# Kernel tuning notes

Hardware: AMD Instinct MI355X
Metric: run time of the kernel (lower is better)

## Reference

```python
import jax, jax.numpy as jnp
import numpy as np
import math

B, P = 4096, 512
WDT = 10          # lyr_wdt = number of irreps (multiplicity)
EPS2 = 1e-12      # NormActivation epsilon=1e-6, squared


def setup_inputs() -> dict:
    key = jax.random.key(0)
    ks = jax.random.split(key, 8)
    return {
        "invar_2b": jax.random.normal(ks[0], (B, P, 5), jnp.float32),
        "vectors_2b": jax.random.normal(ks[1], (B, P, 9), jnp.float32),
        # torch.nn.Linear params (stored as [in, out])
        "w1_0": jax.random.normal(ks[2], (5, WDT), jnp.float32) / math.sqrt(5.0),
        "b1_0": jnp.zeros((WDT,), jnp.float32),
        "w1_1": jax.random.normal(ks[3], (WDT, WDT), jnp.float32) / math.sqrt(float(WDT)),
        "b1_1": jnp.zeros((WDT,), jnp.float32),
        # o3.Linear weights (N(0,1) init, e3nn normalizes by sqrt(mul_in) in forward)
        "lin0_w": jax.random.normal(ks[4], (3, WDT), jnp.float32),
        "na0_b": jnp.zeros((WDT,), jnp.float32),   # NormActivation bias
        "lin1_w": jax.random.normal(ks[5], (WDT, WDT), jnp.float32),
        "na1_b": jnp.zeros((WDT,), jnp.float32),
        "final_w": jax.random.normal(ks[6], (WDT, 1), jnp.float32),
    }


def _self_intrc(x, w, bias):
    """o3.Linear (mul_in x 1o -> mul_out x 1o) + NormActivation(tanh, eps=1e-6, bias).

    x: [B, P, mul_in, 3]
    """
    mul_in = x.shape[-2]
    # single l=1 -> l=1 path; e3nn o3.Linear scales by 1/sqrt(fan_in)
    y = jnp.einsum('bpuc,uw->bpwc', x, w) / jnp.sqrt(jnp.float32(mul_in))
    # NormActivation: norm per irrep, clamped at eps^2 before sqrt
    n = jnp.sqrt(jnp.maximum(jnp.sum(y * y, axis=-1), EPS2))  # [B,P,mul_out]
    s = jnp.tanh(n + bias) / n                                # act(norm+b)/norm
    return y * s[..., None]


def reference(invar_2b, vectors_2b, w1_0, b1_0, w1_1, b1_1,
              lin0_w, na0_b, lin1_w, na1_b, final_w):
    # scalar branch: Linear(5,10) + ReLU, Linear(10,10) + ReLU
    y = jax.nn.relu(invar_2b @ w1_0 + b1_0)
    y = jax.nn.relu(y @ w1_1 + b1_1)              # [B, P, WDT] (10x0e)

    # equivariant branch: two self_intrc blocks on 3x1o -> 10x1o -> 10x1o
    v = vectors_2b.reshape(B, P, 3, 3)            # [B,P,3 irreps,3 comps]
    x = _self_intrc(v, lin0_w, na0_b)             # [B,P,WDT,3]
    x = _self_intrc(x, lin1_w, na1_b)             # [B,P,WDT,3]

    # ElementwiseTensorProduct(10x0e, 10x1o) -> 10x1o: per-irrep scalar gating
    x = y[..., None] * x                          # [B,P,WDT,3]

    # final o3.Linear 10x1o -> 1x1o
    x = jnp.einsum('bpuc,uw->bpwc', x, final_w) / jnp.sqrt(jnp.float32(WDT))
    return jnp.sum(x[..., 0, :], axis=1)          # sum over pairs -> [B, 3]
```

## Files before the change

kernel.cpp:

```cpp
#include <hip/hip_runtime.h>
#include <math.h>

#define BB 4096
#define PP 512
#define WDT 10

typedef float float2v __attribute__((ext_vector_type(2)));

#define PKFMA(a, b, c) __builtin_elementwise_fma(a, b, c)
#define PKMAX(a, b)    __builtin_elementwise_max(a, b)
#define FENCE()        __builtin_amdgcn_sched_barrier(0)

__device__ __forceinline__ float2v bc2(float s) { return (float2v){s, s}; }

__device__ __forceinline__ float fast_tanh(float x) {
    float e = __builtin_amdgcn_exp2f(x * 2.8853900817779268f);
    return 1.0f - 2.0f * __builtin_amdgcn_rcpf(e + 1.0f);
}

__global__ __launch_bounds__(256) void frc_2b_kernel(
    const float* __restrict__ invar,
    const float* __restrict__ vectors,
    const float* __restrict__ w1_0,
    const float* __restrict__ b1_0,
    const float* __restrict__ w1_1,
    const float* __restrict__ b1_1,
    const float* __restrict__ lin0_w,
    const float* __restrict__ na0_b,
    const float* __restrict__ lin1_w,
    const float* __restrict__ na1_b,
    const float* __restrict__ final_w,
    float* __restrict__ out)
{
    __shared__ float red[4][3];

    const int b   = blockIdx.x;
    const int tid = threadIdx.x;

    const float* iv0 = invar   + ((size_t)b * PP + tid) * 5;
    const float* vv0 = vectors + ((size_t)b * PP + tid) * 9;
    float in5a[2][5];
    float v[2][9];
    #pragma unroll
    for (int i = 0; i < 5; ++i) { in5a[0][i] = iv0[i]; in5a[1][i] = iv0[256 * 5 + i]; }
    #pragma unroll
    for (int i = 0; i < 9; ++i) { v[0][i] = vv0[i]; v[1][i] = vv0[256 * 9 + i]; }

    const float k3sq  = 0.33333333333333333f;
    const float k3k10 = 0.18257418583505536f;
    const float k10   = 0.31622776601683794f;
    const float2v z2  = {0.f, 0.f};

    float2v yp[2][5];
    #pragma unroll
    for (int jp = 0; jp < 5; ++jp) {
        float2v bb = *(const float2v*)(b1_0 + 2 * jp);
        yp[0][jp] = bb; yp[1][jp] = bb;
    }
    #pragma unroll
    for (int i = 0; i < 5; ++i) {
        #pragma unroll
        for (int jp = 0; jp < 5; ++jp) {
            float2v wp = *(const float2v*)(w1_0 + i * WDT + 2 * jp);
            yp[0][jp] = PKFMA(wp, bc2(in5a[0][i]), yp[0][jp]);
            yp[1][jp] = PKFMA(wp, bc2(in5a[1][i]), yp[1][jp]);
        }
    }
    #pragma unroll
    for (int pr = 0; pr < 2; ++pr)
        #pragma unroll
        for (int jp = 0; jp < 5; ++jp) yp[pr][jp] = PKMAX(yp[pr][jp], z2);
    FENCE();

    float2v y2p[2][5];
    #pragma unroll
    for (int jp = 0; jp < 5; ++jp) {
        float2v bb = *(const float2v*)(b1_1 + 2 * jp);
        y2p[0][jp] = bb; y2p[1][jp] = bb;
    }
    #pragma unroll
    for (int k = 0; k < 5; ++k) {
        #pragma unroll
        for (int jp = 0; jp < 5; ++jp) {
            float2v wp = *(const float2v*)(w1_1 + k * WDT + 2 * jp);
            y2p[0][jp] = PKFMA(wp, bc2(yp[0][k >> 1][k & 1]), y2p[0][jp]);
            y2p[1][jp] = PKFMA(wp, bc2(yp[1][k >> 1][k & 1]), y2p[1][jp]);
        }
    }
    FENCE();
    #pragma unroll
    for (int k = 5; k < WDT; ++k) {
        #pragma unroll
        for (int jp = 0; jp < 5; ++jp) {
            float2v wp = *(const float2v*)(w1_1 + k * WDT + 2 * jp);
            y2p[0][jp] = PKFMA(wp, bc2(yp[0][k >> 1][k & 1]), y2p[0][jp]);
            y2p[1][jp] = PKFMA(wp, bc2(yp[1][k >> 1][k & 1]), y2p[1][jp]);
        }
    }
    #pragma unroll
    for (int pr = 0; pr < 2; ++pr)
        #pragma unroll
        for (int jp = 0; jp < 5; ++jp) y2p[pr][jp] = PKMAX(y2p[pr][jp], z2);
    FENCE();

    float2v c0p[2][5], c1p[2][5], c2p[2][5];
    #pragma unroll
    for (int pr = 0; pr < 2; ++pr)
        #pragma unroll
        for (int jp = 0; jp < 5; ++jp) { c0p[pr][jp] = z2; c1p[pr][jp] = z2; c2p[pr][jp] = z2; }
    #pragma unroll
    for (int u = 0; u < 3; ++u) {
        #pragma unroll
        for (int jp = 0; jp < 5; ++jp) {
            float2v wp = *(const float2v*)(lin0_w + u * WDT + 2 * jp);
            #pragma unroll
            for (int pr = 0; pr < 2; ++pr) {
                c0p[pr][jp] = PKFMA(wp, bc2(v[pr][u * 3 + 0]), c0p[pr][jp]);
                c1p[pr][jp] = PKFMA(wp, bc2(v[pr][u * 3 + 1]), c1p[pr][jp]);
                c2p[pr][jp] = PKFMA(wp, bc2(v[pr][u * 3 + 2]), c2p[pr][jp]);
            }
        }
    }
    float2v x0p[2][5], x1p[2][5], x2p[2][5];
    #pragma unroll
    for (int jp = 0; jp < 5; ++jp) {
        float2v nab = *(const float2v*)(na0_b + 2 * jp);
        #pragma unroll
        for (int pr = 0; pr < 2; ++pr) {
            float2v n2p = PKFMA(c0p[pr][jp], c0p[pr][jp],
                          PKFMA(c1p[pr][jp], c1p[pr][jp], c2p[pr][jp] * c2p[pr][jp]));
            float2v mp  = PKMAX(n2p * bc2(k3sq), bc2(1e-12f));
            float fh[2];
            #pragma unroll
            for (int h = 0; h < 2; ++h) {
                float m     = mp[h];
                float inv_n = __builtin_amdgcn_rsqf(m);
                float n     = m * inv_n;
                float t     = fast_tanh(n + nab[h]);
                fh[h] = t * inv_n * k3k10;
            }
            float2v fp = {fh[0], fh[1]};
            x0p[pr][jp] = c0p[pr][jp] * fp;
            x1p[pr][jp] = c1p[pr][jp] * fp;
            x2p[pr][jp] = c2p[pr][jp] * fp;
        }
    }
    FENCE();

    float2v e0p[2][5], e1p[2][5], e2p[2][5];
    #pragma unroll
    for (int pr = 0; pr < 2; ++pr)
        #pragma unroll
        for (int jp = 0; jp < 5; ++jp) { e0p[pr][jp] = z2; e1p[pr][jp] = z2; e2p[pr][jp] = z2; }
    #pragma unroll
    for (int u = 0; u < 5; ++u) {
        #pragma unroll
        for (int jp = 0; jp < 5; ++jp) {
            float2v wp = *(const float2v*)(lin1_w + u * WDT + 2 * jp);
            #pragma unroll
            for (int pr = 0; pr < 2; ++pr) {
                e0p[pr][jp] = PKFMA(wp, bc2(x0p[pr][u >> 1][u & 1]), e0p[pr][jp]);
                e1p[pr][jp] = PKFMA(wp, bc2(x1p[pr][u >> 1][u & 1]), e1p[pr][jp]);
                e2p[pr][jp] = PKFMA(wp, bc2(x2p[pr][u >> 1][u & 1]), e2p[pr][jp]);
            }
        }
    }
    FENCE();
    #pragma unroll
    for (int u = 5; u < WDT; ++u) {
        #pragma unroll
        for (int jp = 0; jp < 5; ++jp) {
            float2v wp = *(const float2v*)(lin1_w + u * WDT + 2 * jp);
            #pragma unroll
            for (int pr = 0; pr < 2; ++pr) {
                e0p[pr][jp] = PKFMA(wp, bc2(x0p[pr][u >> 1][u & 1]), e0p[pr][jp]);
                e1p[pr][jp] = PKFMA(wp, bc2(x1p[pr][u >> 1][u & 1]), e1p[pr][jp]);
                e2p[pr][jp] = PKFMA(wp, bc2(x2p[pr][u >> 1][u & 1]), e2p[pr][jp]);
            }
        }
    }
    FENCE();

    float2v a0p = z2, a1p = z2, a2p = z2;
    #pragma unroll
    for (int jp = 0; jp < 5; ++jp) {
        float2v nab = *(const float2v*)(na1_b + 2 * jp);
        float2v fwp = *(const float2v*)(final_w + 2 * jp);
        #pragma unroll
        for (int pr = 0; pr < 2; ++pr) {
            float2v n2p = PKFMA(e0p[pr][jp], e0p[pr][jp],
                          PKFMA(e1p[pr][jp], e1p[pr][jp], e2p[pr][jp] * e2p[pr][jp]));
            float2v mp  = PKMAX(n2p, bc2(1e-12f));
            float gh[2];
            #pragma unroll
            for (int h = 0; h < 2; ++h) {
                float m     = mp[h];
                float inv_n = __builtin_amdgcn_rsqf(m);
                float n     = m * inv_n;
                float t     = fast_tanh(n + nab[h]);
                gh[h] = y2p[pr][jp][h] * t * inv_n * fwp[h];
            }
            float2v gp = {gh[0], gh[1]};
            a0p = PKFMA(e0p[pr][jp], gp, a0p);
            a1p = PKFMA(e1p[pr][jp], gp, a1p);
            a2p = PKFMA(e2p[pr][jp], gp, a2p);
        }
    }
    float acc0 = (a0p[0] + a0p[1]) * k10;
    float acc1 = (a1p[0] + a1p[1]) * k10;
    float acc2 = (a2p[0] + a2p[1]) * k10;

    #pragma unroll
    for (int off = 32; off > 0; off >>= 1) {
        acc0 += __shfl_down(acc0, off, 64);
        acc1 += __shfl_down(acc1, off, 64);
        acc2 += __shfl_down(acc2, off, 64);
    }
    const int wave = tid >> 6;
    if ((tid & 63) == 0) { red[wave][0] = acc0; red[wave][1] = acc1; red[wave][2] = acc2; }
    __syncthreads();
    if (tid == 0) {
        float r0 = 0.f, r1 = 0.f, r2 = 0.f;
        #pragma unroll
        for (int wv = 0; wv < 4; ++wv) { r0 += red[wv][0]; r1 += red[wv][1]; r2 += red[wv][2]; }
        out[b * 3 + 0] = r0;
        out[b * 3 + 1] = r1;
        out[b * 3 + 2] = r2;
    }
}

extern "C" void kernel_launch(void* const* d_in, const int* in_sizes, int n_in,
                              void* d_out, int out_size, void* d_ws, size_t ws_size,
                              hipStream_t stream) {
    const float* invar   = (const float*)d_in[0];
    const float* vectors = (const float*)d_in[1];
    const float* w1_0    = (const float*)d_in[2];
    const float* b1_0    = (const float*)d_in[3];
    const float* w1_1    = (const float*)d_in[4];
    const float* b1_1    = (const float*)d_in[5];
    const float* lin0_w  = (const float*)d_in[6];
    const float* na0_b   = (const float*)d_in[7];
    const float* lin1_w  = (const float*)d_in[8];
    const float* na1_b   = (const float*)d_in[9];
    const float* final_w = (const float*)d_in[10];
    float* out = (float*)d_out;

    frc_2b_kernel<<<BB, 256, 0, stream>>>(invar, vectors, w1_0, b1_0, w1_1, b1_1,
                                          lin0_w, na0_b, lin1_w, na1_b, final_w, out);
}
```

Baseline: 166.4 us.

## Process four contiguous pairs per thread with 128-bit vector loads

Each thread now handles four adjacent pairs instead of two strided ones, and the block shrinks to 128 threads. The contiguous layout lets every thread read its 20 invariant floats and 36 vector floats as float4 loads, which cuts the number of load instructions. The cost is roughly double the per-thread register state, which may lower occupancy. Per-lane 16-byte strided accesses also coalesce less well across a wave.

```diff
diff --git a/kernel.cpp b/kernel.cpp
--- a/kernel.cpp
+++ b/kernel.cpp
@@ -4,8 +4,11 @@
 #define BB 4096
 #define PP 512
 #define WDT 10
+#define NP 4
+#define NT 128
 
 typedef float float2v __attribute__((ext_vector_type(2)));
+typedef float float4v __attribute__((ext_vector_type(4)));
 
 #define PKFMA(a, b, c) __builtin_elementwise_fma(a, b, c)
 #define PKMAX(a, b)    __builtin_elementwise_max(a, b)
@@ -18,7 +21,7 @@
     return 1.0f - 2.0f * __builtin_amdgcn_rcpf(e + 1.0f);
 }
 
-__global__ __launch_bounds__(256) void frc_2b_kernel(
+__global__ __launch_bounds__(NT) void frc_2b_kernel(
     const float* __restrict__ invar,
     const float* __restrict__ vectors,
     const float* __restrict__ w1_0,
@@ -32,59 +35,77 @@
     const float* __restrict__ final_w,
     float* __restrict__ out)
 {
-    __shared__ float red[4][3];
+    __shared__ float red[2][3];
 
     const int b   = blockIdx.x;
     const int tid = threadIdx.x;
 
-    const float* iv0 = invar   + ((size_t)b * PP + tid) * 5;
-    const float* vv0 = vectors + ((size_t)b * PP + tid) * 9;
-    float in5a[2][5];
-    float v[2][9];
-    #pragma unroll
-    for (int i = 0; i < 5; ++i) { in5a[0][i] = iv0[i]; in5a[1][i] = iv0[256 * 5 + i]; }
-    #pragma unroll
-    for (int i = 0; i < 9; ++i) { v[0][i] = vv0[i]; v[1][i] = vv0[256 * 9 + i]; }
+    const float* iv0 = invar   + ((size_t)b * PP + tid * NP) * 5;
+    const float* vv0 = vectors + ((size_t)b * PP + tid * NP) * 9;
+    float in5a[NP][5];
+    float v[NP][9];
+    #pragma unroll
+    for (int q = 0; q < 5; ++q) {
+        float4v f = ((const float4v*)iv0)[q];
+        #pragma unroll
+        for (int r = 0; r < 4; ++r) {
+            int idx = q * 4 + r;
+            in5a[idx / 5][idx % 5] = f[r];
+        }
+    }
+    #pragma unroll
+    for (int q = 0; q < 9; ++q) {
+        float4v f = ((const float4v*)vv0)[q];
+        #pragma unroll
+        for (int r = 0; r < 4; ++r) {
+            int idx = q * 4 + r;
+            v[idx / 9][idx % 9] = f[r];
+        }
+    }
 
     const float k3sq  = 0.33333333333333333f;
     const float k3k10 = 0.18257418583505536f;
     const float k10   = 0.31622776601683794f;
     const float2v z2  = {0.f, 0.f};
 
-    float2v yp[2][5];
+    float2v yp[NP][5];
     #pragma unroll
     for (int jp = 0; jp < 5; ++jp) {
         float2v bb = *(const float2v*)(b1_0 + 2 * jp);
-        yp[0][jp] = bb; yp[1][jp] = bb;
+        #pragma unroll
+        for (int pr = 0; pr < NP; ++pr) yp[pr][jp] = bb;
     }
     #pragma unroll
     for (int i = 0; i < 5; ++i) {
         #pragma unroll
         for (int jp = 0; jp < 5; ++jp) {
             float2v wp = *(const float2v*)(w1_0 + i * WDT + 2 * jp);
-            yp[0][jp] = PKFMA(wp, bc2(in5a[0][i]), yp[0][jp]);
-            yp[1][jp] = PKFMA(wp, bc2(in5a[1][i]), yp[1][jp]);
-        }
-    }
-    #pragma unroll
-    for (int pr = 0; pr < 2; ++pr)
+            #pragma unroll
+            for (int pr = 0; pr < NP; ++pr)
+                yp[pr][jp] = PKFMA(wp, bc2(in5a[pr][i]), yp[pr][jp]);
+        }
+    }
+    #pragma unroll
+    for (int pr = 0; pr < NP; ++pr)
         #pragma unroll
         for (int jp = 0; jp < 5; ++jp) yp[pr][jp] = PKMAX(yp[pr][jp], z2);
     FENCE();
 
-    float2v y2p[2][5];
+    float2v y2p[NP][5];
     #pragma unroll
     for (int jp = 0; jp < 5; ++jp) {
         float2v bb = *(const float2v*)(b1_1 + 2 * jp);
-        y2p[0][jp] = bb; y2p[1][jp] = bb;
+        #pragma unroll
+        for (int pr = 0; pr < NP; ++pr) y2p[pr][jp] = bb;
     }
     #pragma unroll
     for (int k = 0; k < 5; ++k) {
         #pragma unroll
         for (int jp = 0; jp < 5; ++jp) {
             float2v wp = *(const float2v*)(w1_1 + k * WDT + 2 * jp);
-            y2p[0][jp] = PKFMA(wp, bc2(yp[0][k >> 1][k & 1]), y2p[0][jp]);
-            y2p[1][jp] = PKFMA(wp, bc2(yp[1][k >> 1][k & 1]), y2p[1][jp]);
+            #pragma unroll
+            for (int pr = 0; pr < NP; ++pr)
+                y2p[pr][jp] = PKFMA(wp, bc2(yp[pr][k >> 1][k & 1]), y2p[pr][jp]);
         }
     }
     FENCE();
@@ -93,19 +114,20 @@
         #pragma unroll
         for (int jp = 0; jp < 5; ++jp) {
             float2v wp = *(const float2v*)(w1_1 + k * WDT + 2 * jp);
-            y2p[0][jp] = PKFMA(wp, bc2(yp[0][k >> 1][k & 1]), y2p[0][jp]);
-            y2p[1][jp] = PKFMA(wp, bc2(yp[1][k >> 1][k & 1]), y2p[1][jp]);
-        }
-    }
-    #pragma unroll
-    for (int pr = 0; pr < 2; ++pr)
+            #pragma unroll
+            for (int pr = 0; pr < NP; ++pr)
+                y2p[pr][jp] = PKFMA(wp, bc2(yp[pr][k >> 1][k & 1]), y2p[pr][jp]);
+        }
+    }
+    #pragma unroll
+    for (int pr = 0; pr < NP; ++pr)
         #pragma unroll
         for (int jp = 0; jp < 5; ++jp) y2p[pr][jp] = PKMAX(y2p[pr][jp], z2);
     FENCE();
 
-    float2v c0p[2][5], c1p[2][5], c2p[2][5];
-    #pragma unroll
-    for (int pr = 0; pr < 2; ++pr)
+    float2v c0p[NP][5], c1p[NP][5], c2p[NP][5];
+    #pragma unroll
+    for (int pr = 0; pr < NP; ++pr)
         #pragma unroll
         for (int jp = 0; jp < 5; ++jp) { c0p[pr][jp] = z2; c1p[pr][jp] = z2; c2p[pr][jp] = z2; }
     #pragma unroll
@@ -114,19 +136,19 @@
         for (int jp = 0; jp < 5; ++jp) {
             float2v wp = *(const float2v*)(lin0_w + u * WDT + 2 * jp);
             #pragma unroll
-            for (int pr = 0; pr < 2; ++pr) {
+            for (int pr = 0; pr < NP; ++pr) {
                 c0p[pr][jp] = PKFMA(wp, bc2(v[pr][u * 3 + 0]), c0p[pr][jp]);
                 c1p[pr][jp] = PKFMA(wp, bc2(v[pr][u * 3 + 1]), c1p[pr][jp]);
                 c2p[pr][jp] = PKFMA(wp, bc2(v[pr][u * 3 + 2]), c2p[pr][jp]);
             }
         }
     }
-    float2v x0p[2][5], x1p[2][5], x2p[2][5];
+    float2v x0p[NP][5], x1p[NP][5], x2p[NP][5];
     #pragma unroll
     for (int jp = 0; jp < 5; ++jp) {
         float2v nab = *(const float2v*)(na0_b + 2 * jp);
         #pragma unroll
-        for (int pr = 0; pr < 2; ++pr) {
+        for (int pr = 0; pr < NP; ++pr) {
             float2v n2p = PKFMA(c0p[pr][jp], c0p[pr][jp],
                           PKFMA(c1p[pr][jp], c1p[pr][jp], c2p[pr][jp] * c2p[pr][jp]));
             float2v mp  = PKMAX(n2p * bc2(k3sq), bc2(1e-12f));
@@ -147,9 +169,9 @@
     }
     FENCE();
 
-    float2v e0p[2][5], e1p[2][5], e2p[2][5];
-    #pragma unroll
-    for (int pr = 0; pr < 2; ++pr)
+    float2v e0p[NP][5], e1p[NP][5], e2p[NP][5];
+    #pragma unroll
+    for (int pr = 0; pr < NP; ++pr)
         #pragma unroll
         for (int jp = 0; jp < 5; ++jp) { e0p[pr][jp] = z2; e1p[pr][jp] = z2; e2p[pr][jp] = z2; }
     #pragma unroll
@@ -158,7 +180,7 @@
         for (int jp = 0; jp < 5; ++jp) {
             float2v wp = *(const float2v*)(lin1_w + u * WDT + 2 * jp);
             #pragma unroll
-            for (int pr = 0; pr < 2; ++pr) {
+            for (int pr = 0; pr < NP; ++pr) {
                 e0p[pr][jp] = PKFMA(wp, bc2(x0p[pr][u >> 1][u & 1]), e0p[pr][jp]);
                 e1p[pr][jp] = PKFMA(wp, bc2(x1p[pr][u >> 1][u & 1]), e1p[pr][jp]);
                 e2p[pr][jp] = PKFMA(wp, bc2(x2p[pr][u >> 1][u & 1]), e2p[pr][jp]);
@@ -172,7 +194,7 @@
         for (int jp = 0; jp < 5; ++jp) {
             float2v wp = *(const float2v*)(lin1_w + u * WDT + 2 * jp);
             #pragma unroll
-            for (int pr = 0; pr < 2; ++pr) {
+            for (int pr = 0; pr < NP; ++pr) {
                 e0p[pr][jp] = PKFMA(wp, bc2(x0p[pr][u >> 1][u & 1]), e0p[pr][jp]);
                 e1p[pr][jp] = PKFMA(wp, bc2(x1p[pr][u >> 1][u & 1]), e1p[pr][jp]);
                 e2p[pr][jp] = PKFMA(wp, bc2(x2p[pr][u >> 1][u & 1]), e2p[pr][jp]);
@@ -187,7 +209,7 @@
         float2v nab = *(const float2v*)(na1_b + 2 * jp);
         float2v fwp = *(const float2v*)(final_w + 2 * jp);
         #pragma unroll
-        for (int pr = 0; pr < 2; ++pr) {
+        for (int pr = 0; pr < NP; ++pr) {
             float2v n2p = PKFMA(e0p[pr][jp], e0p[pr][jp],
                           PKFMA(e1p[pr][jp], e1p[pr][jp], e2p[pr][jp] * e2p[pr][jp]));
             float2v mp  = PKMAX(n2p, bc2(1e-12f));
@@ -220,12 +242,9 @@
     if ((tid & 63) == 0) { red[wave][0] = acc0; red[wave][1] = acc1; red[wave][2] = acc2; }
     __syncthreads();
     if (tid == 0) {
-        float r0 = 0.f, r1 = 0.f, r2 = 0.f;
-        #pragma unroll
-        for (int wv = 0; wv < 4; ++wv) { r0 += red[wv][0]; r1 += red[wv][1]; r2 += red[wv][2]; }
-        out[b * 3 + 0] = r0;
-        out[b * 3 + 1] = r1;
-        out[b * 3 + 2] = r2;
+        out[b * 3 + 0] = red[0][0] + red[1][0];
+        out[b * 3 + 1] = red[0][1] + red[1][1];
+        out[b * 3 + 2] = red[0][2] + red[1][2];
     }
 }
 
@@ -245,6 +264,6 @@
     const float* final_w = (const float*)d_in[10];
     float* out = (float*)d_out;
 
-    frc_2b_kernel<<<BB, 256, 0, stream>>>(invar, vectors, w1_0, b1_0, w1_1, b1_1,
-                                          lin0_w, na0_b, lin1_w, na1_b, final_w, out);
+    frc_2b_kernel<<<BB, NT, 0, stream>>>(invar, vectors, w1_0, b1_0, w1_1, b1_1,
+                                         lin0_w, na0_b, lin1_w, na1_b, final_w, out);
 }
```

After: 184.5 us. 1.11x slower.
